# Kernel tuning notes

Hardware: AMD Instinct MI355X
Metric: run time of the kernel (lower is better)

Reference implementation:

```python
import jax, jax.numpy as jnp
import numpy as np

HIDDEN = 2048
HEADS = 16
HEAD_DIM = HIDDEN // HEADS
B, S = 4, 2048
NEG_INF = float('-inf')


def setup_inputs() -> dict:
    key = jax.random.key(0)
    ks = jax.random.split(key, 9)
    x = jax.random.normal(ks[0], (B, S, HIDDEN), dtype=jnp.float32)
    # causal mask: 0 on/below diagonal, -inf above (matches masked_fill(mask == -inf))
    causal = jnp.tril(jnp.ones((S, S), dtype=bool))
    mask = jnp.where(causal, 0.0, NEG_INF).astype(jnp.float32)[None, None]
    sc = 1.0 / np.sqrt(HIDDEN)
    Wq = jax.random.normal(ks[1], (HIDDEN, HIDDEN), jnp.float32) * sc
    Wk = jax.random.normal(ks[2], (HIDDEN, HIDDEN), jnp.float32) * sc
    Wv = jax.random.normal(ks[3], (HIDDEN, HIDDEN), jnp.float32) * sc
    Wo = jax.random.normal(ks[4], (HIDDEN, HIDDEN), jnp.float32) * sc
    bq = jax.random.normal(ks[5], (HIDDEN,), jnp.float32) * 0.02
    bk = jax.random.normal(ks[6], (HIDDEN,), jnp.float32) * 0.02
    bv = jax.random.normal(ks[7], (HIDDEN,), jnp.float32) * 0.02
    bo = jax.random.normal(ks[8], (HIDDEN,), jnp.float32) * 0.02
    return {"x": x, "mask": mask, "Wq": Wq, "bq": bq, "Wk": Wk, "bk": bk,
            "Wv": Wv, "bv": bv, "Wo": Wo, "bo": bo}


def reference(x, mask, Wq, bq, Wk, bk, Wv, bv, Wo, bo):
    Bsz, Slen, H = x.shape
    scale = jnp.float32(HEAD_DIM) ** 0.5
    # torch Linear: y = x @ W.T + b
    def proj(W, b):
        y = jnp.einsum('bsh,oh->bso', x, W) + b
        return y.reshape(Bsz, Slen, HEADS, HEAD_DIM).transpose(0, 2, 1, 3)  # [B,H,S,D]
    q = proj(Wq, bq)
    k = proj(Wk, bk)
    v = proj(Wv, bv)
    scores = jnp.einsum('bhqd,bhkd->bhqk', q, k) / scale
    scores = jnp.where(mask == NEG_INF, NEG_INF, scores)
    attn = jax.nn.softmax(scores, axis=-1)  # dropout is identity in eval
    ctx = jnp.einsum('bhqk,bhkd->bhqd', attn, v)
    ctx = ctx.transpose(0, 2, 1, 3).reshape(Bsz, Slen, H)
    return jnp.einsum('bsh,oh->bso', ctx, Wo) + bo
```

## Files before the change

### kernel.cpp

```cpp
#include <hip/hip_runtime.h>
#include <hip/hip_bf16.h>

#define HID 2048
#define NH 16
#define HD 128
#define SQ 2048
#define NB 4

typedef __attribute__((ext_vector_type(8))) short short8;
typedef __attribute__((ext_vector_type(4))) float f32x4;

__device__ __forceinline__ unsigned short f2bf(float f) {
  unsigned int u = __float_as_uint(f);
  u += 0x7fffu + ((u >> 16) & 1u);
  return (unsigned short)(u >> 16);
}
__device__ __forceinline__ unsigned int pkbf(float a, float b) {
  unsigned int ua = __float_as_uint(a) + 0x8000u;
  unsigned int ub = __float_as_uint(b) + 0x8000u;
  return (ua >> 16) | (ub & 0xffff0000u);
}
__device__ __forceinline__ f32x4 mfma16(short8 a, short8 b, f32x4 c) {
  return __builtin_amdgcn_mfma_f32_16x16x32_bf16(a, b, c, 0, 0, 0);
}
__device__ __forceinline__ void dma16(const void* g, void* l) {
  __builtin_amdgcn_global_load_lds(
      (__attribute__((address_space(1))) void*)(uintptr_t)g,
      (__attribute__((address_space(3))) void*)(uintptr_t)l, 16, 0, 0);
}
__device__ __forceinline__ void wgbar() {
  asm volatile("" ::: "memory");
  __builtin_amdgcn_s_barrier();
  asm volatile("" ::: "memory");
}

__global__ __launch_bounds__(256)
void cvt_bf16(const float* __restrict__ X, const float* __restrict__ Wq,
              const float* __restrict__ Wk, const float* __restrict__ Wv,
              const float* __restrict__ Wo, unsigned short* __restrict__ xbf,
              unsigned short* __restrict__ wbf)
{
  const size_t i8 = ((size_t)blockIdx.x * 256 + threadIdx.x) * 8;
  const float* src; unsigned short* dst; size_t off;
  const size_t XEL = (size_t)NB * SQ * HID;
  if (i8 < XEL) { src = X; dst = xbf; off = i8; }
  else {
    size_t t = i8 - XEL;
    int wi = (int)(t >> 22);
    off = t & ((1u << 22) - 1);
    src = (wi == 0) ? Wq : (wi == 1) ? Wk : (wi == 2) ? Wv : Wo;
    dst = wbf + ((size_t)wi << 22);
  }
  f32x4 a = *(const f32x4*)(src + off);
  f32x4 b = *(const f32x4*)(src + off + 4);
  short8 o;
  o[0] = (short)f2bf(a[0]); o[1] = (short)f2bf(a[1]);
  o[2] = (short)f2bf(a[2]); o[3] = (short)f2bf(a[3]);
  o[4] = (short)f2bf(b[0]); o[5] = (short)f2bf(b[1]);
  o[6] = (short)f2bf(b[2]); o[7] = (short)f2bf(b[3]);
  *(short8*)(dst + off) = o;
}

__global__ __launch_bounds__(512, 2)
void proj_gemm(const unsigned short* __restrict__ xbf,
               const unsigned short* __restrict__ wbf,
               const float* __restrict__ bq, const float* __restrict__ bk,
               const float* __restrict__ bv,
               unsigned short* __restrict__ qo, unsigned short* __restrict__ ko,
               unsigned short* __restrict__ vto)
{
  __shared__ unsigned short As[2][2][256 * 32];
  __shared__ unsigned short Bs[2][2][256 * 32];

  const int L = blockIdx.x;
  const int xcd = L & 7, sidx = L >> 3;
  const int mode = sidx >> 5;
  const int r5 = sidx & 31;
  const int mt = xcd * 4 + (r5 & 3);
  const int nt = r5 >> 2;
  const int m0 = mt * 256, n0 = nt * 256;

  const unsigned short* W = wbf + (size_t)mode * (HID * HID);
  const float* bias = (mode == 0) ? bq : (mode == 1) ? bk : bv;

  const int tid = threadIdx.x, lane = tid & 63, wv = tid >> 6;
  const int wm = wv >> 2, wn = wv & 3;
  const int g = lane >> 4, ln = lane & 15;

  const int srow = tid >> 2, scg = (tid & 3) ^ (srow & 3);
  const unsigned short* Ag = xbf + (size_t)(m0 + srow) * HID + scg * 8;
  const unsigned short* Bg = W + (size_t)(n0 + srow) * HID + scg * 8;

  f32x4 acc[8][4];
#pragma unroll
  for (int i = 0; i < 8; ++i)
#pragma unroll
    for (int j = 0; j < 4; ++j) acc[i][j] = (f32x4){0.f, 0.f, 0.f, 0.f};

  const int c8 = (g ^ (ln & 3)) * 8;
  const int arow0 = (wm * 128 + ln) * 32 + c8;
  const int brow0 = (wn * 64 + ln) * 32 + c8;

  auto stA = [&](int bufs, int khs, int kts) {
    const unsigned short* src = Ag + kts * 64 + khs * 32;
#pragma unroll
    for (int rr = 0; rr < 2; ++rr)
      dma16(src + (size_t)(rr * 128) * HID, &As[bufs][khs][rr * 4096 + wv * 512]);
  };
  auto stB = [&](int bufs, int khs, int kts) {
    const unsigned short* src = Bg + kts * 64 + khs * 32;
#pragma unroll
    for (int rr = 0; rr < 2; ++rr)
      dma16(src + (size_t)(rr * 128) * HID, &Bs[bufs][khs][rr * 4096 + wv * 512]);
  };

  stA(0, 0, 0); stB(0, 0, 0);
  stA(0, 1, 0); stB(0, 1, 0);
  stA(1, 0, 1); stB(1, 0, 1);

  for (int I = 0; I < 16; ++I) {
    const bool tail = (I == 15);
#pragma unroll
    for (int p = 0; p < 8; ++p) {
      const int buf = p >> 2, ksub = (p >> 1) & 1, qm = p & 1;
      if ((p & 1) == 0) {
        if (tail) asm volatile("s_waitcnt vmcnt(0)" ::: "memory");
        else      asm volatile("s_waitcnt vmcnt(8)" ::: "memory");
        wgbar();
      }
      short8 af[4], bfr[4];
      const unsigned short* Ab = &As[buf][ksub][0];
      const unsigned short* Bb = &Bs[buf][ksub][0];
#pragma unroll
      for (int ii = 0; ii < 4; ++ii)
        af[ii] = *(const short8*)&Ab[arow0 + (qm * 4 + ii) * 512];
#pragma unroll
      for (int j = 0; j < 4; ++j)
        bfr[j] = *(const short8*)&Bb[brow0 + j * 512];
      {
        const int grp = p >> 1;
        const int kts = 2 * I + 1 + ((grp + 1) >> 1);
        if (kts < 32) {
          const int khs = 1 - (grp & 1);
          const int bufs = kts & 1;
          if ((p & 1) == 0) stA(bufs, khs, kts); else stB(bufs, khs, kts);
        }
      }
      __builtin_amdgcn_s_setprio(1);
#pragma unroll
      for (int ii = 0; ii < 4; ++ii)
#pragma unroll
        for (int j = 0; j < 4; ++j)
          acc[qm * 4 + ii][j] = mfma16(af[ii], bfr[j], acc[qm * 4 + ii][j]);
      __builtin_amdgcn_s_setprio(0);
      if (p & 1) wgbar();
    }
  }

#pragma unroll
  for (int j = 0; j < 4; ++j) {
    const int ng = n0 + wn * 64 + j * 16 + ln;
    const float bb = bias[ng];
    const int h = ng >> 7, d = ng & (HD - 1);
#pragma unroll
    for (int i = 0; i < 8; ++i) {
      const int mg = m0 + wm * 128 + i * 16 + g * 4;
      const int b = mg >> 11, s0 = mg & (SQ - 1);
      if (mode == 2) {
        uint2 o2;
        o2.x = pkbf(acc[i][j][0] + bb, acc[i][j][1] + bb);
        o2.y = pkbf(acc[i][j][2] + bb, acc[i][j][3] + bb);
        *(uint2*)&vto[((size_t)(b * NH + h) * HD + d) * SQ + s0] = o2;
      } else {
        unsigned short* dst = (mode == 1) ? ko : qo;
#pragma unroll
        for (int r = 0; r < 4; ++r)
          dst[((size_t)(b * NH + h) * SQ + (s0 + r)) * HD + d] = f2bf(acc[i][j][r] + bb);
      }
    }
  }
}

__global__ __launch_bounds__(256)
void attn(unsigned short* __restrict__ qc,
          const unsigned short* __restrict__ k,
          const unsigned short* __restrict__ vt)
{
  __shared__ unsigned short Ks[2][32 * 128];
  __shared__ unsigned short Vs[2][128 * 32];
  __shared__ unsigned short Ps[4][32 * 40];

  const int qt = (gridDim.x - 1) - blockIdx.x;
  const int bh = blockIdx.y;
  const int tid = threadIdx.x, lane = tid & 63, w = tid >> 6;
  const int g = lane >> 4, ln = lane & 15;
  const float kScale = 0.12753102543f;

  const int scgK = (tid & 15) ^ (tid >> 4);
  const unsigned short* Kg = k + ((size_t)bh * SQ + (tid >> 4)) * HD + scgK * 8;
  const int scgV = (tid & 3) ^ ((tid >> 4) & 3);
  const unsigned short* Vg = vt + ((size_t)bh * HD + (tid >> 2)) * SQ + scgV * 8;

  short8 qf[2][4];
  const size_t qrow = (size_t)bh * SQ + qt * 128 + w * 32;
#pragma unroll
  for (int n = 0; n < 2; ++n)
#pragma unroll
    for (int ks = 0; ks < 4; ++ks)
      qf[n][ks] = *(const short8*)(qc + (qrow + n * 16 + ln) * HD + ks * 32 + g * 8);

  f32x4 oacc[8][2];
  float lsum[2] = {0.f, 0.f};
#pragma unroll
  for (int jd = 0; jd < 8; ++jd)
#pragma unroll
    for (int n = 0; n < 2; ++n) oacc[jd][n] = (f32x4){0.f, 0.f, 0.f, 0.f};

  const int T = 4 * (qt + 1);
#pragma unroll
  for (int i = 0; i < 2; ++i) {
    dma16(Kg + (size_t)(i * 16) * HD, &Ks[0][(i * 256 + w * 64) * 8]);
    dma16(Vg + (size_t)(i * 64) * SQ, &Vs[0][(i * 256 + w * 64) * 8]);
  }

  for (int t = 0; t < T; ++t) {
    const int cur = t & 1;
    __syncthreads();
    if (t + 1 < T) {
      const int nb = cur ^ 1;
      const int kb = (t + 1) * 32;
#pragma unroll
      for (int i = 0; i < 2; ++i) {
        dma16(Kg + (size_t)(kb + i * 16) * HD, &Ks[nb][(i * 256 + w * 64) * 8]);
        dma16(Vg + (size_t)(i * 64) * SQ + kb, &Vs[nb][(i * 256 + w * 64) * 8]);
      }
    }

    const int dqrel = qt * 128 + w * 32 - t * 32;
    if (dqrel + 31 < 0) continue;
    int jm = ((dqrel + 31) >> 4) + 1; if (jm > 2) jm = 2;
    const bool masked = (dqrel < 31);

    f32x4 sacc[2][2];
#pragma unroll
    for (int j = 0; j < 2; ++j)
#pragma unroll
      for (int n = 0; n < 2; ++n) sacc[j][n] = (f32x4){0.f, 0.f, 0.f, 0.f};
    __builtin_amdgcn_s_setprio(1);
#pragma unroll
    for (int ks = 0; ks < 4; ++ks)
#pragma unroll
      for (int j = 0; j < 2; ++j)
        if (j < jm) {
          short8 kf = *(const short8*)&Ks[cur][(j * 16 + ln) * 128 + (((ks * 4 + g) ^ ln) * 8)];
          sacc[j][0] = mfma16(kf, qf[0][ks], sacc[j][0]);
          sacc[j][1] = mfma16(kf, qf[1][ks], sacc[j][1]);
        }
    __builtin_amdgcn_s_setprio(0);

#pragma unroll
    for (int j = 0; j < 2; ++j) {
      const int km = j * 16 + g * 4;
#pragma unroll
      for (int n = 0; n < 2; ++n) {
        f32x4 s4 = sacc[j][n];
        float e0 = exp2f(s4[0] * kScale);
        float e1 = exp2f(s4[1] * kScale);
        float e2 = exp2f(s4[2] * kScale);
        float e3 = exp2f(s4[3] * kScale);
        if (masked) {
          const int qm = dqrel + n * 16 + ln;
          if (km + 0 > qm) e0 = 0.f;
          if (km + 1 > qm) e1 = 0.f;
          if (km + 2 > qm) e2 = 0.f;
          if (km + 3 > qm) e3 = 0.f;
        }
        lsum[n] += (e0 + e1) + (e2 + e3);
        uint2 p2; p2.x = pkbf(e0, e1); p2.y = pkbf(e2, e3);
        *(uint2*)&Ps[w][(n * 16 + ln) * 40 + j * 16 + g * 4] = p2;
      }
    }

    short8 pf0 = *(const short8*)&Ps[w][ln * 40 + g * 8];
    short8 pf1 = *(const short8*)&Ps[w][(16 + ln) * 40 + g * 8];
    __builtin_amdgcn_s_setprio(1);
#pragma unroll
    for (int jd = 0; jd < 8; ++jd) {
      short8 vf = *(const short8*)&Vs[cur][(jd * 16 + ln) * 32 + ((g ^ (ln >> 2)) * 8)];
      oacc[jd][0] = mfma16(vf, pf0, oacc[jd][0]);
      oacc[jd][1] = mfma16(vf, pf1, oacc[jd][1]);
    }
    __builtin_amdgcn_s_setprio(0);
  }

#pragma unroll
  for (int n = 0; n < 2; ++n) {
    float l = lsum[n];
    l += __shfl_xor(l, 16);
    l += __shfl_xor(l, 32);
    const float inv = 1.f / l;
    unsigned short* orow = qc + (qrow + n * 16 + ln) * HD;
#pragma unroll
    for (int jd = 0; jd < 8; ++jd) {
      uint2 o2;
      o2.x = pkbf(oacc[jd][n][0] * inv, oacc[jd][n][1] * inv);
      o2.y = pkbf(oacc[jd][n][2] * inv, oacc[jd][n][3] * inv);
      *(uint2*)(orow + jd * 16 + g * 4) = o2;
    }
  }
}

__global__ __launch_bounds__(512, 2)
void out_gemm(const unsigned short* __restrict__ qc,
              const unsigned short* __restrict__ wobf,
              const float* __restrict__ bo, float* __restrict__ out)
{
  __shared__ unsigned short As[2][2][256 * 32];
  __shared__ unsigned short Bs[2][2][256 * 32];

  const int L = blockIdx.x;
  const int xcd = L & 7, r5 = L >> 3;
  const int mt = xcd * 4 + (r5 & 3);
  const int nt = r5 >> 2;
  const int m0 = mt * 256, n0 = nt * 256;

  const int tid = threadIdx.x, lane = tid & 63, wv = tid >> 6;
  const int wm = wv >> 2, wn = wv & 3;
  const int g = lane >> 4, ln = lane & 15;

  const int srow = tid >> 2, scg = (tid & 3) ^ (srow & 3);
  const int bI16 = (m0 >> 11) * 16;
  const int sbase = (m0 & (SQ - 1)) + srow;
  const unsigned short* Bg = wobf + (size_t)(n0 + srow) * HID + scg * 8;

  f32x4 acc[8][4];
#pragma unroll
  for (int i = 0; i < 8; ++i)
#pragma unroll
    for (int j = 0; j < 4; ++j) acc[i][j] = (f32x4){0.f, 0.f, 0.f, 0.f};

  const int c8 = (g ^ (ln & 3)) * 8;
  const int arow0 = (wm * 128 + ln) * 32 + c8;
  const int brow0 = (wn * 64 + ln) * 32 + c8;

  auto stA = [&](int bufs, int khs, int kts) {
    const unsigned short* src = qc + ((size_t)(bI16 + (kts >> 1)) * SQ + sbase) * HD
                                + (kts & 1) * 64 + khs * 32 + scg * 8;
#pragma unroll
    for (int rr = 0; rr < 2; ++rr)
      dma16(src + (size_t)(rr * 128) * HD, &As[bufs][khs][rr * 4096 + wv * 512]);
  };
  auto stB = [&](int bufs, int khs, int kts) {
    const unsigned short* src = Bg + kts * 64 + khs * 32;
#pragma unroll
    for (int rr = 0; rr < 2; ++rr)
      dma16(src + (size_t)(rr * 128) * HID, &Bs[bufs][khs][rr * 4096 + wv * 512]);
  };

  stA(0, 0, 0); stB(0, 0, 0);
  stA(0, 1, 0); stB(0, 1, 0);
  stA(1, 0, 1); stB(1, 0, 1);

  for (int I = 0; I < 16; ++I) {
    const bool tail = (I == 15);
#pragma unroll
    for (int p = 0; p < 8; ++p) {
      const int buf = p >> 2, ksub = (p >> 1) & 1, qm = p & 1;
      if ((p & 1) == 0) {
        if (tail) asm volatile("s_waitcnt vmcnt(0)" ::: "memory");
        else      asm volatile("s_waitcnt vmcnt(8)" ::: "memory");
        wgbar();
      }
      short8 af[4], bfr[4];
      const unsigned short* Ab = &As[buf][ksub][0];
      const unsigned short* Bb = &Bs[buf][ksub][0];
#pragma unroll
      for (int ii = 0; ii < 4; ++ii)
        af[ii] = *(const short8*)&Ab[arow0 + (qm * 4 + ii) * 512];
#pragma unroll
      for (int j = 0; j < 4; ++j)
        bfr[j] = *(const short8*)&Bb[brow0 + j * 512];
      {
        const int grp = p >> 1;
        const int kts = 2 * I + 1 + ((grp + 1) >> 1);
        if (kts < 32) {
          const int khs = 1 - (grp & 1);
          const int bufs = kts & 1;
          if ((p & 1) == 0) stA(bufs, khs, kts); else stB(bufs, khs, kts);
        }
      }
      __builtin_amdgcn_s_setprio(1);
#pragma unroll
      for (int ii = 0; ii < 4; ++ii)
#pragma unroll
        for (int j = 0; j < 4; ++j)
          acc[qm * 4 + ii][j] = mfma16(af[ii], bfr[j], acc[qm * 4 + ii][j]);
      __builtin_amdgcn_s_setprio(0);
      if (p & 1) wgbar();
    }
  }

#pragma unroll
  for (int j = 0; j < 4; ++j) {
    const int ng = n0 + wn * 64 + j * 16 + ln;
    const float bb = bo[ng];
#pragma unroll
    for (int i = 0; i < 8; ++i) {
      const int mg = m0 + wm * 128 + i * 16 + g * 4;
#pragma unroll
      for (int r = 0; r < 4; ++r)
        out[(size_t)(mg + r) * HID + ng] = acc[i][j][r] + bb;
    }
  }
}

extern "C" void kernel_launch(void* const* d_in, const int* in_sizes, int n_in,
                              void* d_out, int out_size, void* d_ws, size_t ws_size,
                              hipStream_t stream) {
  const float* x  = (const float*)d_in[0];
  const float* Wq = (const float*)d_in[2];
  const float* bq = (const float*)d_in[3];
  const float* Wk = (const float*)d_in[4];
  const float* bk = (const float*)d_in[5];
  const float* Wv = (const float*)d_in[6];
  const float* bv = (const float*)d_in[7];
  const float* Wo = (const float*)d_in[8];
  const float* bo = (const float*)d_in[9];
  float* out = (float*)d_out;

  const size_t WEL = (size_t)HID * HID;
  const size_t PER = (size_t)NB * NH * SQ * HD;
  unsigned short* wbf = (unsigned short*)d_ws;
  unsigned short* qw  = wbf + 4 * WEL;
  unsigned short* kw  = qw + PER;
  unsigned short* vtw = kw + PER;
  unsigned short* xbf = (unsigned short*)d_out;

  cvt_bf16<<<16384, 256, 0, stream>>>(x, Wq, Wk, Wv, Wo, xbf, wbf);

  proj_gemm<<<768, 512, 0, stream>>>(xbf, wbf, bq, bk, bv, qw, kw, vtw);

  attn<<<dim3(SQ / 128, NB * NH), 256, 0, stream>>>(qw, kw, vtw);

  out_gemm<<<256, 512, 0, stream>>>(qw, wbf + 3 * WEL, bo, out);
}
```

Measured before the change: 660.7 us.

## Enlarge attention tiles and triple-buffer K/V loads with XCD-aware block mapping

The attention kernel now uses 512-thread blocks, each covering 256 query rows with 64-key tiles. It triple-buffers K/V async copies, using explicit vmcnt waits and a workgroup barrier instead of double-buffering with syncthreads. Blocks are remapped so that heads are grouped by XCD and causal tiles are scheduled longest-first. The goal is more MFMA work per barrier, deeper load/compute overlap and better L2 locality, at the cost of more LDS and registers per block, which may reduce occupancy.

```diff
diff --git a/kernel.cpp b/kernel.cpp
--- a/kernel.cpp
+++ b/kernel.cpp
@@ -181,33 +181,54 @@
   }
 }
 
-__global__ __launch_bounds__(256)
+__global__ __launch_bounds__(512, 2)
 void attn(unsigned short* __restrict__ qc,
           const unsigned short* __restrict__ k,
           const unsigned short* __restrict__ vt)
 {
-  __shared__ unsigned short Ks[2][32 * 128];
-  __shared__ unsigned short Vs[2][128 * 32];
-  __shared__ unsigned short Ps[4][32 * 40];
-
-  const int qt = (gridDim.x - 1) - blockIdx.x;
-  const int bh = blockIdx.y;
+  __shared__ unsigned short Ks[3][64 * 128];
+  __shared__ unsigned short Vs[3][128 * 64];
+  __shared__ unsigned short Ps[8][32 * 72];
+
+  const int L = blockIdx.x;
+  const int xcd = L & 7;
+  const int qt = 7 - ((L >> 3) & 7);
+  const int bh = xcd + 8 * (L >> 6);
   const int tid = threadIdx.x, lane = tid & 63, w = tid >> 6;
   const int g = lane >> 4, ln = lane & 15;
   const float kScale = 0.12753102543f;
 
-  const int scgK = (tid & 15) ^ (tid >> 4);
-  const unsigned short* Kg = k + ((size_t)bh * SQ + (tid >> 4)) * HD + scgK * 8;
-  const int scgV = (tid & 3) ^ ((tid >> 4) & 3);
-  const unsigned short* Vg = vt + ((size_t)bh * HD + (tid >> 2)) * SQ + scgV * 8;
+  const int krow = w * 4 + (lane >> 4);
+  const int kchunk = lane & 15;
+  const int vrow = w * 8 + (lane >> 3);
+  const int vchunk = lane & 7;
 
   short8 qf[2][4];
-  const size_t qrow = (size_t)bh * SQ + qt * 128 + w * 32;
+  const size_t qrow = (size_t)bh * SQ + qt * 256 + w * 32;
 #pragma unroll
   for (int n = 0; n < 2; ++n)
 #pragma unroll
     for (int ks = 0; ks < 4; ++ks)
       qf[n][ks] = *(const short8*)(qc + (qrow + n * 16 + ln) * HD + ks * 32 + g * 8);
+  asm volatile("" :: "v"(qf[0][0]), "v"(qf[0][1]), "v"(qf[0][2]), "v"(qf[0][3]),
+                    "v"(qf[1][0]), "v"(qf[1][1]), "v"(qf[1][2]), "v"(qf[1][3]));
+
+  auto stK = [&](int buf, int t) {
+#pragma unroll
+    for (int i = 0; i < 2; ++i) {
+      const int r = i * 32 + krow;
+      dma16(k + ((size_t)bh * SQ + t * 64 + r) * HD + ((kchunk ^ (r & 15)) * 8),
+            &Ks[buf][(i * 32 + w * 4) * 128]);
+    }
+  };
+  auto stV = [&](int buf, int t) {
+#pragma unroll
+    for (int i = 0; i < 2; ++i) {
+      const int r = i * 64 + vrow;
+      dma16(vt + ((size_t)bh * HD + r) * SQ + t * 64 + ((vchunk ^ (r & 7)) * 8),
+            &Vs[buf][(i * 64 + w * 8) * 64]);
+    }
+  };
 
   f32x4 oacc[8][2];
   float lsum[2] = {0.f, 0.f};
@@ -217,80 +238,84 @@
     for (int n = 0; n < 2; ++n) oacc[jd][n] = (f32x4){0.f, 0.f, 0.f, 0.f};
 
   const int T = 4 * (qt + 1);
-#pragma unroll
-  for (int i = 0; i < 2; ++i) {
-    dma16(Kg + (size_t)(i * 16) * HD, &Ks[0][(i * 256 + w * 64) * 8]);
-    dma16(Vg + (size_t)(i * 64) * SQ, &Vs[0][(i * 256 + w * 64) * 8]);
-  }
-
+  stK(0, 0); stV(0, 0);
+  stK(1, 1); stV(1, 1);
+
+  int cur = 0;
   for (int t = 0; t < T; ++t) {
-    const int cur = t & 1;
-    __syncthreads();
-    if (t + 1 < T) {
-      const int nb = cur ^ 1;
-      const int kb = (t + 1) * 32;
-#pragma unroll
-      for (int i = 0; i < 2; ++i) {
-        dma16(Kg + (size_t)(kb + i * 16) * HD, &Ks[nb][(i * 256 + w * 64) * 8]);
-        dma16(Vg + (size_t)(i * 64) * SQ + kb, &Vs[nb][(i * 256 + w * 64) * 8]);
-      }
-    }
-
-    const int dqrel = qt * 128 + w * 32 - t * 32;
-    if (dqrel + 31 < 0) continue;
-    int jm = ((dqrel + 31) >> 4) + 1; if (jm > 2) jm = 2;
-    const bool masked = (dqrel < 31);
-
-    f32x4 sacc[2][2];
-#pragma unroll
-    for (int j = 0; j < 2; ++j)
-#pragma unroll
-      for (int n = 0; n < 2; ++n) sacc[j][n] = (f32x4){0.f, 0.f, 0.f, 0.f};
-    __builtin_amdgcn_s_setprio(1);
-#pragma unroll
-    for (int ks = 0; ks < 4; ++ks)
-#pragma unroll
-      for (int j = 0; j < 2; ++j)
-        if (j < jm) {
-          short8 kf = *(const short8*)&Ks[cur][(j * 16 + ln) * 128 + (((ks * 4 + g) ^ ln) * 8)];
-          sacc[j][0] = mfma16(kf, qf[0][ks], sacc[j][0]);
-          sacc[j][1] = mfma16(kf, qf[1][ks], sacc[j][1]);
+    if (t + 1 < T) asm volatile("s_waitcnt vmcnt(4)" ::: "memory");
+    else           asm volatile("s_waitcnt vmcnt(0)" ::: "memory");
+    wgbar();
+    if (t + 2 < T) {
+      int nb = cur + 2; if (nb >= 3) nb -= 3;
+      stK(nb, t + 2); stV(nb, t + 2);
+    }
+
+    const int dqrel = qt * 256 + w * 32 - t * 64;
+    if (dqrel + 31 >= 0) {
+      int jm = ((dqrel + 31) >> 4) + 1; if (jm > 4) jm = 4;
+      const bool masked = (dqrel < 63);
+
+      f32x4 sacc[4][2];
+#pragma unroll
+      for (int j = 0; j < 4; ++j)
+#pragma unroll
+        for (int n = 0; n < 2; ++n) sacc[j][n] = (f32x4){0.f, 0.f, 0.f, 0.f};
+      __builtin_amdgcn_s_setprio(1);
+#pragma unroll
+      for (int ks = 0; ks < 4; ++ks)
+#pragma unroll
+        for (int j = 0; j < 4; ++j)
+          if (j < jm) {
+            short8 kf = *(const short8*)&Ks[cur][(j * 16 + ln) * 128 + (((ks * 4 + g) ^ ln) * 8)];
+            sacc[j][0] = mfma16(kf, qf[0][ks], sacc[j][0]);
+            sacc[j][1] = mfma16(kf, qf[1][ks], sacc[j][1]);
+          }
+      __builtin_amdgcn_s_setprio(0);
+
+#pragma unroll
+      for (int j = 0; j < 4; ++j) {
+        const int km = j * 16 + g * 4;
+#pragma unroll
+        for (int n = 0; n < 2; ++n) {
+          f32x4 s4 = sacc[j][n];
+          float e0 = exp2f(s4[0] * kScale);
+          float e1 = exp2f(s4[1] * kScale);
+          float e2 = exp2f(s4[2] * kScale);
+          float e3 = exp2f(s4[3] * kScale);
+          if (masked) {
+            const int qm = dqrel + n * 16 + ln;
+            if (km + 0 > qm) e0 = 0.f;
+            if (km + 1 > qm) e1 = 0.f;
+            if (km + 2 > qm) e2 = 0.f;
+            if (km + 3 > qm) e3 = 0.f;
+          }
+          lsum[n] += (e0 + e1) + (e2 + e3);
+          uint2 p2; p2.x = pkbf(e0, e1); p2.y = pkbf(e2, e3);
+          *(uint2*)&Ps[w][(n * 16 + ln) * 72 + j * 16 + g * 4] = p2;
         }
-    __builtin_amdgcn_s_setprio(0);
-
-#pragma unroll
-    for (int j = 0; j < 2; ++j) {
-      const int km = j * 16 + g * 4;
-#pragma unroll
-      for (int n = 0; n < 2; ++n) {
-        f32x4 s4 = sacc[j][n];
-        float e0 = exp2f(s4[0] * kScale);
-        float e1 = exp2f(s4[1] * kScale);
-        float e2 = exp2f(s4[2] * kScale);
-        float e3 = exp2f(s4[3] * kScale);
-        if (masked) {
-          const int qm = dqrel + n * 16 + ln;
-          if (km + 0 > qm) e0 = 0.f;
-          if (km + 1 > qm) e1 = 0.f;
-          if (km + 2 > qm) e2 = 0.f;
-          if (km + 3 > qm) e3 = 0.f;
+      }
+
+      short8 pa00 = *(const short8*)&Ps[w][ln * 72 + g * 8];
+      short8 pa10 = *(const short8*)&Ps[w][(16 + ln) * 72 + g * 8];
+      short8 pa01 = *(const short8*)&Ps[w][ln * 72 + 32 + g * 8];
+      short8 pa11 = *(const short8*)&Ps[w][(16 + ln) * 72 + 32 + g * 8];
+      const bool hi = (jm > 2);
+      __builtin_amdgcn_s_setprio(1);
+#pragma unroll
+      for (int jd = 0; jd < 8; ++jd) {
+        short8 vfa = *(const short8*)&Vs[cur][(jd * 16 + ln) * 64 + ((g ^ (ln & 7)) * 8)];
+        oacc[jd][0] = mfma16(vfa, pa00, oacc[jd][0]);
+        oacc[jd][1] = mfma16(vfa, pa10, oacc[jd][1]);
+        if (hi) {
+          short8 vfb = *(const short8*)&Vs[cur][(jd * 16 + ln) * 64 + (((4 + g) ^ (ln & 7)) * 8)];
+          oacc[jd][0] = mfma16(vfb, pa01, oacc[jd][0]);
+          oacc[jd][1] = mfma16(vfb, pa11, oacc[jd][1]);
         }
-        lsum[n] += (e0 + e1) + (e2 + e3);
-        uint2 p2; p2.x = pkbf(e0, e1); p2.y = pkbf(e2, e3);
-        *(uint2*)&Ps[w][(n * 16 + ln) * 40 + j * 16 + g * 4] = p2;
-      }
-    }
-
-    short8 pf0 = *(const short8*)&Ps[w][ln * 40 + g * 8];
-    short8 pf1 = *(const short8*)&Ps[w][(16 + ln) * 40 + g * 8];
-    __builtin_amdgcn_s_setprio(1);
-#pragma unroll
-    for (int jd = 0; jd < 8; ++jd) {
-      short8 vf = *(const short8*)&Vs[cur][(jd * 16 + ln) * 32 + ((g ^ (ln >> 2)) * 8)];
-      oacc[jd][0] = mfma16(vf, pf0, oacc[jd][0]);
-      oacc[jd][1] = mfma16(vf, pf1, oacc[jd][1]);
-    }
-    __builtin_amdgcn_s_setprio(0);
+      }
+      __builtin_amdgcn_s_setprio(0);
+    }
+    cur = (cur == 2) ? 0 : cur + 1;
   }
 
 #pragma unroll
@@ -440,7 +465,7 @@
 
   proj_gemm<<<768, 512, 0, stream>>>(xbf, wbf, bq, bk, bv, qw, kw, vtw);
 
-  attn<<<dim3(SQ / 128, NB * NH), 256, 0, stream>>>(qw, kw, vtw);
+  attn<<<512, 512, 0, stream>>>(qw, kw, vtw);
 
   out_gemm<<<256, 512, 0, stream>>>(qw, wbf + 3 * WEL, bo, out);
 }
```

Result: no change. 654.6 us (-0.9%).
